# Kernel tuning notes

Measured on AMD Instinct MI355X. Metric: run time of the kernel, lower is better.

The kernel has to match this reference:

```python
import jax, jax.numpy as jnp
import numpy as np
from jax import lax

DN = ('NCHW', 'OIHW', 'NCHW')


def setup_inputs() -> dict:
    key = jax.random.key(0)
    k1, k2, k3, k4, k5, k6 = jax.random.split(key, 6)
    B, Ch, H, W = 16, 256, 32, 32   # two feature maps of 256 ch -> c = 512
    C = 2 * Ch
    return {
        'x1': jax.random.normal(k1, (B, Ch, H, W), dtype=jnp.float32),
        'x2': jax.random.normal(k2, (B, Ch, H, W), dtype=jnp.float32),
        'g_w': jax.random.normal(k3, (C, C, 3, 3), dtype=jnp.float32) * 0.02,
        'w_w': jax.random.normal(k4, (256, C, 1, 1), dtype=jnp.float32) * 0.05,
        'weight1': jax.random.normal(k5, (C, 16), dtype=jnp.float32) * 0.1,
        'weight2': jax.random.normal(k6, (C, 16), dtype=jnp.float32) * 0.1,
    }


def reference(x1, x2, g_w, w_w, weight1, weight2):
    x = jnp.concatenate([x1, x2], axis=1)            # [b, c, h, w]
    b, c, h, w = x.shape
    g_x = lax.conv_general_dilated(x, g_w, (1, 1), 'SAME', dimension_numbers=DN)
    value = g_x.reshape(b, c, h * w)                 # [b, c, n]
    q = x.reshape(b, c, h * w)                       # query == key source
    sim = jnp.einsum('bcn,bdn->bcd', q, q) * (float(c) ** -0.5)  # [b, c, c]
    random_map = weight1 @ weight2.T                 # [c, c]
    attn = jax.nn.softmax(sim + random_map[None], axis=-1)
    ctx = jnp.einsum('bcd,bdn->bcn', attn, value).reshape(b, c, h, w)
    out = lax.conv_general_dilated(ctx, w_w, (1, 1), 'VALID', dimension_numbers=DN)
    return out
```

## Files before the change

kernel.cpp:

```cpp
#include <hip/hip_runtime.h>
#include <math.h>

typedef float f32x4 __attribute__((ext_vector_type(4)));
typedef short s16x8 __attribute__((ext_vector_type(8)));
typedef unsigned int u32;
typedef unsigned short u16;
typedef u16 u16x4 __attribute__((ext_vector_type(4)));

static constexpr size_t OFF_XT    = 0;
static constexpr size_t OFF_XQ    = 4734976;
static constexpr size_t OFF_ATTNT = 4734976;
static constexpr size_t OFF_WATTN = 6832128;
static constexpr size_t OFF_P0    = 8929280;
static constexpr size_t OFF_P1    = 11026432;
static constexpr size_t OFF_VT    = 8929280;
static constexpr size_t OFF_WA    = 13123584;
static constexpr size_t OFF_RM    = 14303232;
static constexpr size_t OFF_WWB   = 14565376;

__device__ __forceinline__ u16 f2bf(float f) {
    u32 u = __float_as_uint(f);
    u32 r = (u + 0x7FFFu + ((u >> 16) & 1u)) >> 16;
    return (u16)r;
}
__device__ __forceinline__ float bf2f(u16 v) {
    return __uint_as_float(((u32)v) << 16);
}

__device__ __forceinline__ void gload_lds16(const void* g, void* l) {
    __builtin_amdgcn_global_load_lds(
        (const u32 __attribute__((address_space(1)))*)(uintptr_t)g,
        (u32 __attribute__((address_space(3)))*)(uintptr_t)l, 16, 0, 0);
}

__global__ __launch_bounds__(256) void prep_kernel(const float* __restrict__ x1,
                                                   const float* __restrict__ x2,
                                                   const float* __restrict__ gw,
                                                   const float* __restrict__ ww,
                                                   const float* __restrict__ w1,
                                                   const float* __restrict__ w2,
                                                   float* __restrict__ rm,
                                                   u16* __restrict__ wA,
                                                   u16* __restrict__ wwb,
                                                   u16* __restrict__ xT,
                                                   u16* __restrict__ xq) {
    __shared__ __attribute__((aligned(16))) u32 shm[4608];
    const int t = threadIdx.x;
    const int bid = blockIdx.x;

    if (bid < 512) {
        const int co = bid;
        const float* g = gw + (size_t)co * 4608;
        float* lf = (float*)shm;
#pragma unroll
        for (int i = 0; i < 18; ++i) lf[t + i * 256] = g[t + i * 256];
        __syncthreads();
        u16* dst = wA + (size_t)co * 4608;
#pragma unroll
        for (int i = 0; i < 18; ++i) {
            int k = t + i * 256;
            int r = k >> 9, ci = k & 511;
            dst[k] = f2bf(lf[ci * 9 + r]);
        }
    } else if (bid < 2560) {
        int xid = bid - 512;
        int nt = xid & 15;
        int cit = (xid >> 4) & 7;
        int b = xid >> 7;
        int n0 = nt * 64, ci0 = cit * 64;
        const float* src = (ci0 < 256) ? (x1 + ((size_t)(b * 256 + ci0)) * 1024)
                                       : (x2 + ((size_t)(b * 256 + ci0 - 256)) * 1024);
        u16* xqb = xq + ((size_t)(b * 512 + ci0)) * 1024;
        u16* lt = (u16*)shm;
#pragma unroll
        for (int p4 = 0; p4 < 4; ++p4) {
            int ch = (t >> 4) + p4 * 16;
            int px = (t & 15) * 4;
            float4 v = *(const float4*)&src[(size_t)ch * 1024 + n0 + px];
            u16x4 pk = {f2bf(v.x), f2bf(v.y), f2bf(v.z), f2bf(v.w)};
            *(u16x4*)&xqb[(size_t)ch * 1024 + n0 + px] = pk;
            lt[(px + 0) * 65 + ch] = pk[0];
            lt[(px + 1) * 65 + ch] = pk[1];
            lt[(px + 2) * 65 + ch] = pk[2];
            lt[(px + 3) * 65 + ch] = pk[3];
        }
        __syncthreads();
        {
            int px_l = t >> 2, c16 = (t & 3) * 16;
            int n = n0 + px_l;
            int y = n >> 5, x = n & 31;
            int p = (y + 1) * 34 + (x + 1);
            u16* dst = xT + ((size_t)b * 1156 + p) * 512 + ci0 + c16;
            *(s16x8*)&dst[0] = *(const s16x8*)&lt[px_l * 65 + c16];
            *(s16x8*)&dst[8] = *(const s16x8*)&lt[px_l * 65 + c16 + 8];
        }
    } else if (bid < 2576) {
        int b = bid - 2560;
        u16* base = xT + (size_t)b * 1156 * 512;
        s16x8 z = {0, 0, 0, 0, 0, 0, 0, 0};
        for (int idx = t; idx < 132 * 64; idx += 256) {
            int row = idx >> 6, seg = idx & 63;
            int p;
            if (row < 34) p = row;
            else if (row < 68) p = 1122 + (row - 34);
            else if (row < 100) p = (row - 67) * 34;
            else p = (row - 99) * 34 + 33;
            *(s16x8*)&base[(size_t)p * 512 + seg * 8] = z;
        }
    } else if (bid < 3600) {
        int idx = (bid - 2576) * 256 + t;
        int c = idx >> 9, d = idx & 511;
        float s = 0.f;
#pragma unroll
        for (int k = 0; k < 16; ++k) s = fmaf(w1[c * 16 + k], w2[d * 16 + k], s);
        rm[idx] = s;
    } else {
        int idx = (bid - 3600) * 256 + t;
        float4 v = ((const float4*)ww)[idx];
        u16x4 pk = {f2bf(v.x), f2bf(v.y), f2bf(v.z), f2bf(v.w)};
        *(u16x4*)&wwb[(size_t)idx * 4] = pk;
    }
}

__global__ __launch_bounds__(256) void sim_part(const u16* __restrict__ xq,
                                                u16* __restrict__ simP) {
    __shared__ __attribute__((aligned(16))) u16 smem[128 * 128];
    u16* As = smem;
    u16* Bs = smem + 128 * 64;
    const int flat = blockIdx.x;
    const int xcd = flat & 7, slot = flat >> 3;
    const int b = 2 * xcd + (slot >> 5);
    const int r0 = slot & 31;
    const int khalf = r0 >> 4;
    const int s = r0 & 15;
    const int m0 = (s >> 2) * 128, n0 = (s & 3) * 128;
    const int t = threadIdx.x, w = t >> 6, l = t & 63;
    const u16* xb = xq + (size_t)b * 512 * 1024 + khalf * 512;

    const u16 *agp[4], *bgp[4];
    u16 *ald[4], *bld[4];
#pragma unroll
    for (int i = 0; i < 4; ++i) {
        int rr = w * 8 + i * 32 + (l >> 3);
        int gi = (l & 7) ^ (rr & 7);
        agp[i] = xb + (size_t)(m0 + rr) * 1024 + gi * 8;
        bgp[i] = xb + (size_t)(n0 + rr) * 1024 + gi * 8;
        ald[i] = &As[(w * 8 + i * 32) * 64];
        bld[i] = &Bs[(w * 8 + i * 32) * 64];
    }

    f32x4 acc[4][4] = {};
    const int wm = (w >> 1) * 64, wn = (w & 1) * 64;

    for (int kt = 0; kt < 8; ++kt) {
        int ko = kt << 6;
        if (kt) __syncthreads();
#pragma unroll
        for (int i = 0; i < 4; ++i) gload_lds16(agp[i] + ko, ald[i]);
#pragma unroll
        for (int i = 0; i < 4; ++i) gload_lds16(bgp[i] + ko, bld[i]);
        __syncthreads();
#pragma unroll
        for (int kk = 0; kk < 2; ++kk) {
            int gbase = kk * 4 + (l >> 4);
            s16x8 af[4], bf[4];
#pragma unroll
            for (int i = 0; i < 4; ++i) {
                int row = wm + i * 16 + (l & 15);
                af[i] = *(const s16x8*)&As[row * 64 + ((gbase ^ (row & 7)) << 3)];
            }
#pragma unroll
            for (int j = 0; j < 4; ++j) {
                int row = wn + j * 16 + (l & 15);
                bf[j] = *(const s16x8*)&Bs[row * 64 + ((gbase ^ (row & 7)) << 3)];
            }
#pragma unroll
            for (int i = 0; i < 4; ++i)
#pragma unroll
                for (int j = 0; j < 4; ++j)
                    acc[i][j] = __builtin_amdgcn_mfma_f32_16x16x32_bf16(af[i], bf[j], acc[i][j], 0, 0, 0);
        }
    }

    __syncthreads();
    const int col = l & 15, r4 = (l >> 4) * 4;
#pragma unroll
    for (int i = 0; i < 4; ++i)
#pragma unroll
        for (int j = 0; j < 4; ++j) {
            int n_l = wn + j * 16 + col;
            int m_b = wm + i * 16 + r4;
            u16x4 pk = {f2bf(acc[i][j][0]), f2bf(acc[i][j][1]),
                        f2bf(acc[i][j][2]), f2bf(acc[i][j][3])};
            *(u16x4*)&smem[n_l * 128 + (m_b ^ ((n_l & 15) << 3))] = pk;
        }
    __syncthreads();
    u16* sTb = simP + (size_t)khalf * 4194304 + (size_t)b * 512 * 512;
    {
        int n_l = t >> 1;
#pragma unroll
        for (int rep = 0; rep < 8; ++rep) {
            int c0 = (((t & 1) + rep * 2) << 3);
            s16x8 v = *(const s16x8*)&smem[n_l * 128 + (c0 ^ ((n_l & 15) << 3))];
            *(s16x8*)&sTb[(size_t)(n0 + n_l) * 512 + m0 + c0] = v;
        }
    }
}

__global__ __launch_bounds__(256) void finish_kernel(const u16* __restrict__ p0,
                                                     const u16* __restrict__ p1,
                                                     const float* __restrict__ rm,
                                                     u16* __restrict__ attnT) {
    __shared__ float rml[32 * 513];
    __shared__ float scr[256];
    const int t = threadIdx.x;
    const int b = blockIdx.x >> 4, c0 = (blockIdx.x & 15) * 32;
    const int cl = t & 31, g = t >> 5;
    const float scale = 0.04419417382415922f;

    for (int idx = t; idx < 32 * 512; idx += 256) {
        int c_l = idx >> 9, d = idx & 511;
        rml[c_l * 513 + d] = rm[(size_t)(c0 + c_l) * 512 + d];
    }
    __syncthreads();

    const u16* q0 = p0 + (size_t)b * 262144 + c0 + cl;
    const u16* q1 = p1 + (size_t)b * 262144 + c0 + cl;
    u16* ap = attnT + (size_t)b * 262144 + c0 + cl;
    const float* rp = &rml[cl * 513];

    float e[64];
    float s = 0.f;
#pragma unroll
    for (int dd = 0; dd < 64; ++dd) {
        int d = g * 64 + dd;
        float v = (bf2f(q0[(size_t)d * 512]) + bf2f(q1[(size_t)d * 512])) * scale + rp[d];
        e[dd] = __expf(v);
        s += e[dd];
    }
    scr[t] = s;
    __syncthreads();
    float tot = 0.f;
#pragma unroll
    for (int k = 0; k < 8; ++k) tot += scr[k * 32 + cl];
    float inv = 1.f / tot;
#pragma unroll
    for (int dd = 0; dd < 64; ++dd) {
        int d = g * 64 + dd;
        ap[(size_t)d * 512] = f2bf(e[dd] * inv);
    }
}

__global__ __launch_bounds__(256) void conv_gemm(const u16* __restrict__ wA,
                                                 const u16* __restrict__ xT,
                                                 u16* __restrict__ vT) {
    __shared__ __attribute__((aligned(16))) u16 smem[128 * 128];
    u16* As = smem;
    u16* Bs = smem + 128 * 64;
    const int b = blockIdx.z, m0 = blockIdx.y * 128, n0 = blockIdx.x * 128;
    const int t = threadIdx.x, w = t >> 6, l = t & 63;
    const u16* xTb = xT + (size_t)b * 1156 * 512;

    int gi[4], pb[4];
    const u16* agp[4];
    u16 *ald[4], *bld[4];
#pragma unroll
    for (int i = 0; i < 4; ++i) {
        int rr = w * 8 + i * 32 + (l >> 3);
        gi[i] = (l & 7) ^ (rr & 7);
        agp[i] = wA + (size_t)(m0 + rr) * 4608 + gi[i] * 8;
        int n = n0 + rr;
        pb[i] = (n >> 5) * 34 + (n & 31);
        ald[i] = &As[(w * 8 + i * 32) * 64];
        bld[i] = &Bs[(w * 8 + i * 32) * 64];
    }

    f32x4 acc[4][4] = {};
    const int wm = (w >> 1) * 64, wn = (w & 1) * 64;

    for (int kt = 0; kt < 72; ++kt) {
        int r = kt >> 3, ci0k = (kt & 7) << 6;
        int rdiv3 = (r * 11) >> 5;
        int poff = rdiv3 * 34 + (r - rdiv3 * 3);
        int aofs = r * 512 + ci0k;
        if (kt) __syncthreads();
#pragma unroll
        for (int i = 0; i < 4; ++i) gload_lds16(agp[i] + aofs, ald[i]);
#pragma unroll
        for (int i = 0; i < 4; ++i)
            gload_lds16(xTb + (size_t)(pb[i] + poff) * 512 + ci0k + gi[i] * 8, bld[i]);
        __syncthreads();

#pragma unroll
        for (int kk = 0; kk < 2; ++kk) {
            int gbase = kk * 4 + (l >> 4);
            s16x8 af[4], bf[4];
#pragma unroll
            for (int i = 0; i < 4; ++i) {
                int row = wm + i * 16 + (l & 15);
                af[i] = *(const s16x8*)&As[row * 64 + ((gbase ^ (row & 7)) << 3)];
            }
#pragma unroll
            for (int j = 0; j < 4; ++j) {
                int row = wn + j * 16 + (l & 15);
                bf[j] = *(const s16x8*)&Bs[row * 64 + ((gbase ^ (row & 7)) << 3)];
            }
#pragma unroll
            for (int i = 0; i < 4; ++i)
#pragma unroll
                for (int j = 0; j < 4; ++j)
                    acc[i][j] = __builtin_amdgcn_mfma_f32_16x16x32_bf16(af[i], bf[j], acc[i][j], 0, 0, 0);
        }
    }

    __syncthreads();
    const int col = l & 15, r4 = (l >> 4) * 4;
#pragma unroll
    for (int i = 0; i < 4; ++i)
#pragma unroll
        for (int j = 0; j < 4; ++j) {
            int n_l = wn + j * 16 + col;
            int co_b = wm + i * 16 + r4;
            u16x4 pk = {f2bf(acc[i][j][0]), f2bf(acc[i][j][1]),
                        f2bf(acc[i][j][2]), f2bf(acc[i][j][3])};
            *(u16x4*)&smem[n_l * 128 + (co_b ^ ((n_l & 15) << 3))] = pk;
        }
    __syncthreads();
    u16* vTb = vT + (size_t)b * 1024 * 512;
    {
        int n_l = t >> 1;
#pragma unroll
        for (int rep = 0; rep < 8; ++rep) {
            int c0 = (((t & 1) + rep * 2) << 3);
            s16x8 v = *(const s16x8*)&smem[n_l * 128 + (c0 ^ ((n_l & 15) << 3))];
            *(s16x8*)&vTb[(size_t)(n0 + n_l) * 512 + m0 + c0] = v;
        }
    }
}

template <int MODE>
__global__ __launch_bounds__(256) void gemm_nt(const u16* __restrict__ A, size_t sA,
                                               const u16* __restrict__ B, size_t sB,
                                               void* __restrict__ Cv, size_t sC,
                                               int K, int ldc, int mt, int nt) {
    __shared__ __attribute__((aligned(16))) u16 As[128 * 64];
    __shared__ __attribute__((aligned(16))) u16 Bs[128 * 64];
    const int flat = blockIdx.x;
    const int xcd = flat & 7;
    const u32 slot = (u32)(flat >> 3);
    const u32 T = (u32)(mt * nt);
    const int b = 2 * xcd + (int)(slot / T);
    const u32 s = slot % T;
    const int m0 = (int)(s / (u32)nt) * 128, n0 = (int)(s % (u32)nt) * 128;
    const int t = threadIdx.x, w = t >> 6, l = t & 63;
    const u16* Ab = A + (size_t)b * sA;
    const u16* Bb = B + (size_t)b * sB;

    const u16 *agp[4], *bgp[4];
    u16 *ald[4], *bld[4];
#pragma unroll
    for (int i = 0; i < 4; ++i) {
        int rr = w * 8 + i * 32 + (l >> 3);
        int gi = (l & 7) ^ (rr & 7);
        agp[i] = Ab + (size_t)(m0 + rr) * K + gi * 8;
        bgp[i] = Bb + (size_t)(n0 + rr) * K + gi * 8;
        ald[i] = &As[(w * 8 + i * 32) * 64];
        bld[i] = &Bs[(w * 8 + i * 32) * 64];
    }

    f32x4 acc[4][4] = {};
    const int wm = (w >> 1) * 64, wn = (w & 1) * 64;
    const int nkt = K >> 6;
    for (int kt = 0; kt < nkt; ++kt) {
        int ko = kt << 6;
        if (kt) __syncthreads();
#pragma unroll
        for (int i = 0; i < 4; ++i) gload_lds16(agp[i] + ko, ald[i]);
#pragma unroll
        for (int i = 0; i < 4; ++i) gload_lds16(bgp[i] + ko, bld[i]);
        __syncthreads();
#pragma unroll
        for (int kk = 0; kk < 2; ++kk) {
            int gbase = kk * 4 + (l >> 4);
            s16x8 af[4], bf[4];
#pragma unroll
            for (int i = 0; i < 4; ++i) {
                int row = wm + i * 16 + (l & 15);
                af[i] = *(const s16x8*)&As[row * 64 + ((gbase ^ (row & 7)) << 3)];
            }
#pragma unroll
            for (int j = 0; j < 4; ++j) {
                int row = wn + j * 16 + (l & 15);
                bf[j] = *(const s16x8*)&Bs[row * 64 + ((gbase ^ (row & 7)) << 3)];
            }
#pragma unroll
            for (int i = 0; i < 4; ++i)
#pragma unroll
                for (int j = 0; j < 4; ++j)
                    acc[i][j] = __builtin_amdgcn_mfma_f32_16x16x32_bf16(af[i], bf[j], acc[i][j], 0, 0, 0);
        }
    }

    const int col = l & 15, r4 = (l >> 4) * 4;
#pragma unroll
    for (int i = 0; i < 4; ++i)
#pragma unroll
        for (int j = 0; j < 4; ++j)
#pragma unroll
            for (int reg = 0; reg < 4; ++reg) {
                int m = m0 + wm + i * 16 + r4 + reg;
                int n = n0 + wn + j * 16 + col;
                if (MODE == 1) {
                    u16* C = (u16*)Cv + (size_t)b * sC;
                    C[(size_t)m * ldc + n] = f2bf(acc[i][j][reg]);
                } else {
                    float* C = (float*)Cv + (size_t)b * sC;
                    C[(size_t)m * ldc + n] = acc[i][j][reg];
                }
            }
}

extern "C" void kernel_launch(void* const* d_in, const int* in_sizes, int n_in,
                              void* d_out, int out_size, void* d_ws, size_t ws_size,
                              hipStream_t stream) {
    (void)in_sizes; (void)n_in; (void)out_size; (void)ws_size;
    const float* x1 = (const float*)d_in[0];
    const float* x2 = (const float*)d_in[1];
    const float* gw = (const float*)d_in[2];
    const float* ww = (const float*)d_in[3];
    const float* w1 = (const float*)d_in[4];
    const float* w2 = (const float*)d_in[5];
    float* out = (float*)d_out;
    float* ws = (float*)d_ws;

    u16* xT    = (u16*)(ws + OFF_XT);
    u16* xq    = (u16*)(ws + OFF_XQ);
    u16* attnT = (u16*)(ws + OFF_ATTNT);
    u16* wattn = (u16*)(ws + OFF_WATTN);
    u16* simP  = (u16*)(ws + OFF_P0);
    u16* p0    = (u16*)(ws + OFF_P0);
    u16* p1    = (u16*)(ws + OFF_P1);
    u16* vT    = (u16*)(ws + OFF_VT);
    u16* wA    = (u16*)(ws + OFF_WA);
    float* rm  = ws + OFF_RM;
    u16* wwb   = (u16*)(ws + OFF_WWB);

    prep_kernel<<<3728, 256, 0, stream>>>(x1, x2, gw, ww, w1, w2, rm, wA, wwb, xT, xq);
    sim_part<<<512, 256, 0, stream>>>(xq, simP);
    finish_kernel<<<256, 256, 0, stream>>>(p0, p1, rm, attnT);
    gemm_nt<1><<<128, 256, 0, stream>>>(
        wwb, 0, attnT, (size_t)512 * 512, wattn, (size_t)256 * 512, 512, 512, 2, 4);
    conv_gemm<<<dim3(8, 4, 16), 256, 0, stream>>>(wA, xT, vT);
    gemm_nt<2><<<256, 256, 0, stream>>>(
        wattn, (size_t)256 * 512, vT, (size_t)1024 * 512, out, (size_t)256 * 1024, 512, 1024, 2, 8);
}
```

Baseline: 222.5 us.

## Enlarge conv GEMM tile to 256x128 with XCD-aware batch mapping

Raises the implicit-GEMM conv tile from 128x128 to 256x128, so each block loads more weight rows per input tile. This halves the grid to 256 blocks and cuts redundant loads of the im2col input operand. It also remaps the flat block index so that each XCD handles two batches, for L2 locality. In exchange it doubles the accumulator registers to 128 floats per thread and uses 64KB of LDS, which lowers occupancy to roughly one block per CU and leaves only one wave of blocks across 256 CUs.

```diff
diff --git a/kernel.cpp b/kernel.cpp
--- a/kernel.cpp
+++ b/kernel.cpp
@@ -251,32 +251,38 @@
     }
 }
 
-__global__ __launch_bounds__(256) void conv_gemm(const u16* __restrict__ wA,
-                                                 const u16* __restrict__ xT,
-                                                 u16* __restrict__ vT) {
-    __shared__ __attribute__((aligned(16))) u16 smem[128 * 128];
+__global__ __launch_bounds__(256) void conv_gemm2(const u16* __restrict__ wA,
+                                                  const u16* __restrict__ xT,
+                                                  u16* __restrict__ vT) {
+    __shared__ __attribute__((aligned(16))) u16 smem[32768];
     u16* As = smem;
-    u16* Bs = smem + 128 * 64;
-    const int b = blockIdx.z, m0 = blockIdx.y * 128, n0 = blockIdx.x * 128;
+    u16* Bs = smem + 16384;
+    const int flat = blockIdx.x;
+    const int xcd = flat & 7, slot = flat >> 3;
+    const int b = 2 * xcd + (slot >> 4);
+    const int s = slot & 15;
+    const int m0 = (s >> 3) * 256, n0 = (s & 7) * 128;
     const int t = threadIdx.x, w = t >> 6, l = t & 63;
     const u16* xTb = xT + (size_t)b * 1156 * 512;
 
-    int gi[4], pb[4];
-    const u16* agp[4];
-    u16 *ald[4], *bld[4];
+    const u16* agp[8];
+    int giB[4], pb[4];
+#pragma unroll
+    for (int i = 0; i < 8; ++i) {
+        int rr = w * 8 + i * 32 + (l >> 3);
+        int gi = (l & 7) ^ (rr & 7);
+        agp[i] = wA + (size_t)(m0 + rr) * 4608 + gi * 8;
+    }
 #pragma unroll
     for (int i = 0; i < 4; ++i) {
         int rr = w * 8 + i * 32 + (l >> 3);
-        gi[i] = (l & 7) ^ (rr & 7);
-        agp[i] = wA + (size_t)(m0 + rr) * 4608 + gi[i] * 8;
         int n = n0 + rr;
         pb[i] = (n >> 5) * 34 + (n & 31);
-        ald[i] = &As[(w * 8 + i * 32) * 64];
-        bld[i] = &Bs[(w * 8 + i * 32) * 64];
-    }
-
-    f32x4 acc[4][4] = {};
-    const int wm = (w >> 1) * 64, wn = (w & 1) * 64;
+        giB[i] = (l & 7) ^ (rr & 7);
+    }
+
+    f32x4 acc[8][4] = {};
+    const int wm = (w >> 1) * 128, wn = (w & 1) * 64;
 
     for (int kt = 0; kt < 72; ++kt) {
         int r = kt >> 3, ci0k = (kt & 7) << 6;
@@ -285,54 +291,56 @@
         int aofs = r * 512 + ci0k;
         if (kt) __syncthreads();
 #pragma unroll
-        for (int i = 0; i < 4; ++i) gload_lds16(agp[i] + aofs, ald[i]);
+        for (int i = 0; i < 8; ++i)
+            gload_lds16(agp[i] + aofs, &As[(w * 8 + i * 32) * 64]);
 #pragma unroll
         for (int i = 0; i < 4; ++i)
-            gload_lds16(xTb + (size_t)(pb[i] + poff) * 512 + ci0k + gi[i] * 8, bld[i]);
+            gload_lds16(xTb + (size_t)(pb[i] + poff) * 512 + ci0k + giB[i] * 8,
+                        &Bs[(w * 8 + i * 32) * 64]);
         __syncthreads();
 
 #pragma unroll
         for (int kk = 0; kk < 2; ++kk) {
             int gbase = kk * 4 + (l >> 4);
-            s16x8 af[4], bf[4];
-#pragma unroll
-            for (int i = 0; i < 4; ++i) {
-                int row = wm + i * 16 + (l & 15);
-                af[i] = *(const s16x8*)&As[row * 64 + ((gbase ^ (row & 7)) << 3)];
-            }
-#pragma unroll
-            for (int j = 0; j < 4; ++j) {
-                int row = wn + j * 16 + (l & 15);
-                bf[j] = *(const s16x8*)&Bs[row * 64 + ((gbase ^ (row & 7)) << 3)];
-            }
-#pragma unroll
-            for (int i = 0; i < 4; ++i)
-#pragma unroll
-                for (int j = 0; j < 4; ++j)
-                    acc[i][j] = __builtin_amdgcn_mfma_f32_16x16x32_bf16(af[i], bf[j], acc[i][j], 0, 0, 0);
+            s16x8 af[8], bf[4];
+#pragma unroll
+            for (int mi = 0; mi < 8; ++mi) {
+                int row = wm + mi * 16 + (l & 15);
+                af[mi] = *(const s16x8*)&As[row * 64 + ((gbase ^ (row & 7)) << 3)];
+            }
+#pragma unroll
+            for (int q = 0; q < 4; ++q) {
+                int row = wn + q * 16 + (l & 15);
+                bf[q] = *(const s16x8*)&Bs[row * 64 + ((gbase ^ (row & 7)) << 3)];
+            }
+#pragma unroll
+            for (int mi = 0; mi < 8; ++mi)
+#pragma unroll
+                for (int q = 0; q < 4; ++q)
+                    acc[mi][q] = __builtin_amdgcn_mfma_f32_16x16x32_bf16(af[mi], bf[q], acc[mi][q], 0, 0, 0);
         }
     }
 
     __syncthreads();
     const int col = l & 15, r4 = (l >> 4) * 4;
 #pragma unroll
-    for (int i = 0; i < 4; ++i)
-#pragma unroll
-        for (int j = 0; j < 4; ++j) {
-            int n_l = wn + j * 16 + col;
-            int co_b = wm + i * 16 + r4;
-            u16x4 pk = {f2bf(acc[i][j][0]), f2bf(acc[i][j][1]),
-                        f2bf(acc[i][j][2]), f2bf(acc[i][j][3])};
-            *(u16x4*)&smem[n_l * 128 + (co_b ^ ((n_l & 15) << 3))] = pk;
+    for (int mi = 0; mi < 8; ++mi)
+#pragma unroll
+        for (int q = 0; q < 4; ++q) {
+            int n_l = wn + q * 16 + col;
+            int co_b = wm + mi * 16 + r4;
+            u16x4 pk = {f2bf(acc[mi][q][0]), f2bf(acc[mi][q][1]),
+                        f2bf(acc[mi][q][2]), f2bf(acc[mi][q][3])};
+            *(u16x4*)&smem[n_l * 256 + (co_b ^ ((n_l & 15) << 3))] = pk;
         }
     __syncthreads();
     u16* vTb = vT + (size_t)b * 1024 * 512;
     {
         int n_l = t >> 1;
 #pragma unroll
-        for (int rep = 0; rep < 8; ++rep) {
+        for (int rep = 0; rep < 16; ++rep) {
             int c0 = (((t & 1) + rep * 2) << 3);
-            s16x8 v = *(const s16x8*)&smem[n_l * 128 + (c0 ^ ((n_l & 15) << 3))];
+            s16x8 v = *(const s16x8*)&smem[n_l * 256 + (c0 ^ ((n_l & 15) << 3))];
             *(s16x8*)&vTb[(size_t)(n0 + n_l) * 512 + m0 + c0] = v;
         }
     }
@@ -450,7 +458,7 @@
     finish_kernel<<<256, 256, 0, stream>>>(p0, p1, rm, attnT);
     gemm_nt<1><<<128, 256, 0, stream>>>(
         wwb, 0, attnT, (size_t)512 * 512, wattn, (size_t)256 * 512, 512, 512, 2, 4);
-    conv_gemm<<<dim3(8, 4, 16), 256, 0, stream>>>(wA, xT, vT);
+    conv_gemm2<<<256, 256, 0, stream>>>(wA, xT, vT);
     gemm_nt<2><<<256, 256, 0, stream>>>(
         wattn, (size_t)256 * 512, vT, (size_t)1024 * 512, out, (size_t)256 * 1024, 512, 1024, 2, 8);
 }
```

Result: slower. 249.9 us (+12.3%).
